# Performance work log

Hardware: AMD Instinct MI355X
Metric: run time of the kernel (lower is better)

Reference implementation:

```python
import jax, jax.numpy as jnp
import numpy as np
import math

B, T, D = 4, 2048, 1024
N, D_OUT = 1024, 1024
EPS_A = 1e-4
PROJ_BOUND = 1.0


def setup_inputs() -> dict:
    key = jax.random.key(0)
    ks = jax.random.split(key, 4)
    # reset_parameters: rho=0.99, delta0=1.0
    rho, delta0 = 0.99, 1.0
    alpha0 = -math.log(rho) / delta0
    alpha_log_val = math.log(math.expm1(alpha0))
    delta_bias_val = math.log(math.expm1(delta0))
    return {
        "u": jax.random.normal(ks[0], (B, T, D), dtype=jnp.float32),
        "z0": jnp.zeros((B, N), dtype=jnp.float32),
        "W_in_raw": 0.02 * jax.random.normal(ks[1], (N, D), dtype=jnp.float32),
        "W_out_raw": 0.02 * jax.random.normal(ks[2], (D_OUT, N), dtype=jnp.float32),
        "pn_w": 0.02 * jax.random.normal(ks[3], (3 * N, D), dtype=jnp.float32),
        "pn_b": jnp.zeros((3 * N,), dtype=jnp.float32),
        "alpha_log": jnp.full((N,), alpha_log_val, dtype=jnp.float32),
        "delta_bias": jnp.full((N,), delta_bias_val, dtype=jnp.float32),
        "log_gamma": jnp.float32(0.0),
    }


def _bounded_linear(x, W, bound):
    # y = x @ (W/scale)^T with ||W/scale||_2 <= bound (exact spectral norm)
    sigma = jnp.maximum(jnp.linalg.norm(W, ord=2), 1e-5)
    scale = jnp.maximum(sigma / bound, 1.0)
    return x @ (W / scale).T


def reference(u, z0, W_in_raw, W_out_raw, pn_w, pn_b, alpha_log, delta_bias, log_gamma):
    g = jnp.exp(log_gamma)
    u_scaled = g * _bounded_linear(u, W_in_raw, PROJ_BOUND)        # (B,T,N)
    raw = u @ pn_w.T + pn_b                                        # (B,T,3N)
    delta_raw, b_raw, c_raw = jnp.split(raw, 3, axis=-1)
    delta = jax.nn.softplus(delta_raw + delta_bias)
    alpha = jax.nn.softplus(alpha_log)                             # (N,)
    a = jnp.minimum(jnp.exp(-delta * alpha), 1.0 - EPS_A)          # (B,T,N)
    b = jnp.tanh(b_raw)
    c = jnp.tanh(c_raw)
    # exact spectral norm of [[a,b],[c,0]] per coordinate
    p = a * a + c * c
    r = b * b
    q = a * b
    disc = (p - r) * (p - r) + 4.0 * q * q
    lam_max = 0.5 * (p + r + jnp.sqrt(disc + 1e-12))
    sigma = jnp.sqrt(lam_max + 1e-12)
    scale = jnp.maximum(sigma, 1.0)
    a, b, c = a / scale, b / scale, c / scale
    # diagonal recurrence z_{t+1} = a_t * z_t + b_t * u_scaled_t via associative scan
    bu = b * u_scaled
    bu = bu.at[:, 0].add(a[:, 0] * z0)
    def combine(x, y):
        a1, b1 = x
        a2, b2 = y
        return (a2 * a1, a2 * b1 + b2)
    _, z_next = jax.lax.associative_scan(combine, (a, bu), axis=1)  # z_1..z_T (B,T,N)
    # y_t = W_out (c_t * z_t) with z_t = state BEFORE update (one-step delay)
    states = jnp.concatenate([z0[:, None, :], z_next[:, :-1, :]], axis=1)  # z_0..z_{T-1}
    y_hat = c * states
    y = _bounded_linear(y_hat, W_out_raw, PROJ_BOUND)              # (B,T,D_out)
    return y
```

## Files before the change

kernel.cpp:

```cpp
#include <hip/hip_runtime.h>
#include <stdint.h>

#define B_ 4
#define T_ 2048
#define D_ 1024
#define N_ 1024
#define TC 16
#define NCH (T_/TC)
#define SQN 6

typedef __attribute__((ext_vector_type(4))) float f32x4;
typedef __attribute__((ext_vector_type(8))) short bf16x8;
typedef __attribute__((ext_vector_type(4))) unsigned short us4;

__device__ __forceinline__ unsigned short f2bf(float f){
  unsigned int u = __float_as_uint(f);
  return (unsigned short)((u + 0x7fffu + ((u >> 16) & 1u)) >> 16);
}
__device__ __forceinline__ float bf2f(unsigned short h){
  return __uint_as_float(((unsigned int)h) << 16);
}

__device__ __forceinline__ float inv_scale(const float* __restrict__ sc, int z){
  float ll = 0.f, w = 1.f, t = 1.f;
  #pragma unroll
  for (int i = 0; i <= SQN; i++){
    t = sc[8 + 2*i + z];
    ll += w * __logf(t);
    w *= 0.5f;
  }
  float F = sc[8 + 2*(SQN+1) + z];
  ll += w * __logf(F / (t*t));
  float sig = fmaxf(__expf(0.5f * ll), 1e-5f);
  return 1.f / fmaxf(sig, 1.f);
}

__device__ __forceinline__ float softplusf(float x){
  return (x > 0.f) ? (x + __logf(1.f + __expf(-x))) : __logf(1.f + __expf(x));
}
__device__ __forceinline__ float tanhfastf(float x){
  float e = __expf(2.f * x);
  return 1.f - 2.f/(e + 1.f);
}
__device__ __forceinline__ float tanhrcpf(float x){
  float e = __expf(2.f * x);
  return 1.f - 2.f*__builtin_amdgcn_rcpf(e + 1.f);
}

#define U4    2097152
#define WIN4   262144
#define PNW4   786432
#define WOUT4  262144
#define CONV_BLOCKS ((U4 + WIN4 + PNW4 + WOUT4 + 255)/256)

__global__ void k_convert_all(const float* __restrict__ u, const float* __restrict__ Win,
                              const float* __restrict__ pnw, const float* __restrict__ Wout,
                              unsigned short* __restrict__ u16, unsigned short* __restrict__ Wcat16,
                              unsigned short* __restrict__ Wout16, float* __restrict__ sc){
  if (blockIdx.x == 0 && threadIdx.x < 64) sc[threadIdx.x] = 0.f;
  long i = (long)blockIdx.x * 256 + threadIdx.x;
  const float* src; long o; size_t didx; unsigned short* dbuf;
  if (i < U4){
    src = u; o = i; dbuf = u16; didx = (size_t)o;
  } else if (i < U4+WIN4){
    o = i - U4; src = Win;
    int n = (int)(o >> 8), c4 = (int)(o & 255);
    dbuf = Wcat16; didx = (size_t)(4*n)*256 + c4;
  } else if (i < U4+WIN4+PNW4){
    o = i - (U4+WIN4); src = pnw;
    int m = (int)(o >> 8), c4 = (int)(o & 255);
    int s = (m >> 10) + 1, n = m & 1023;
    dbuf = Wcat16; didx = (size_t)(4*n + s)*256 + c4;
  } else if (i < U4+WIN4+PNW4+WOUT4){
    o = i - (U4+WIN4+PNW4); src = Wout; dbuf = Wout16; didx = (size_t)o;
  } else return;
  float4 v = ((const float4*)src)[o];
  us4 w;
  w.x = f2bf(v.x); w.y = f2bf(v.y); w.z = f2bf(v.z); w.w = f2bf(v.w);
  ((us4*)dbuf)[didx] = w;
}

__device__ __forceinline__ void load_lds16(const unsigned short* g, unsigned short* l){
  __builtin_amdgcn_global_load_lds((const __attribute__((address_space(1))) void*)g,
                                   (__attribute__((address_space(3))) void*)l, 16, 0, 0);
}

__global__ __launch_bounds__(256) void k_pgemm(
    const unsigned short* __restrict__ A,
    const unsigned short* __restrict__ Bmat,
    const float* __restrict__ alog, const float* __restrict__ dbias,
    const float* __restrict__ pnb, const float* __restrict__ lgam,
    const float* __restrict__ sc,
    unsigned int* __restrict__ G1,
    float* __restrict__ G2,
    float* __restrict__ Asum, float* __restrict__ Ssum)
{
  __shared__ alignas(16) char smem[36864];
  unsigned short* As = (unsigned short*)smem;
  unsigned short* Bs = (unsigned short*)(smem + 16384);
  const int tid = threadIdx.x;
  const int wid = tid >> 6;
  const int lane = tid & 63;
  const int bn = blockIdx.x, bm = blockIdx.y;
  const int K = 1024;

  const int wr = wid >> 1, wc = wid & 1;
  const int rg = lane >> 3;
  const int cby = (lane & 7) << 4;
  const int srow0 = wid * 32;
  const int frow = lane & 15;
  const int kgrp = lane >> 4;

  const unsigned short* ap[4];
  const unsigned short* bp[4];
  unsigned short* adst[4];
  unsigned short* bdst[4];
  #pragma unroll
  for (int i = 0; i < 4; i++){
    int r = srow0 + i*8 + rg;
    int cb = cby ^ ((r & 7) << 4);
    ap[i] = A    + (size_t)(bm*128 + r)*K + (cb >> 1);
    bp[i] = Bmat + (size_t)(bn*128 + r)*K + (cb >> 1);
    adst[i] = As + (srow0 + i*8)*64;
    bdst[i] = Bs + (srow0 + i*8)*64;
  }
  int aoff[4][2], boff[4][2];
  #pragma unroll
  for (int m = 0; m < 4; m++){
    int r = wr*64 + m*16 + frow;
    #pragma unroll
    for (int kk = 0; kk < 2; kk++)
      aoff[m][kk] = r*128 + ((kk*64 + kgrp*16) ^ ((r & 7) << 4));
  }
  #pragma unroll
  for (int n2 = 0; n2 < 4; n2++){
    int r = wc*64 + n2*16 + frow;
    #pragma unroll
    for (int kk = 0; kk < 2; kk++)
      boff[n2][kk] = r*128 + ((kk*64 + kgrp*16) ^ ((r & 7) << 4));
  }

  f32x4 acc[4][4] = {};

  for (int kt = 0; kt < K; kt += 64){
    #pragma unroll
    for (int i = 0; i < 4; i++){
      load_lds16(ap[i], adst[i]);
      load_lds16(bp[i], bdst[i]);
      ap[i] += 64; bp[i] += 64;
    }
    __syncthreads();
    #pragma unroll
    for (int kk = 0; kk < 2; kk++){
      bf16x8 af[4], bfv[4];
      #pragma unroll
      for (int m = 0; m < 4; m++)
        af[m] = *(const bf16x8*)((const char*)As + aoff[m][kk]);
      #pragma unroll
      for (int n2 = 0; n2 < 4; n2++)
        bfv[n2] = *(const bf16x8*)((const char*)Bs + boff[n2][kk]);
      #pragma unroll
      for (int m = 0; m < 4; m++)
        #pragma unroll
        for (int n2 = 0; n2 < 4; n2++)
          acc[m][n2] = __builtin_amdgcn_mfma_f32_16x16x32_bf16(bfv[n2], af[m], acc[m][n2], 0, 0, 0);
    }
    __syncthreads();
  }

  unsigned int* g1s = (unsigned int*)smem;
  float*        g2s = (float*)(smem + 18432);

  const float ginv = __expf(lgam[0]) * inv_scale(sc, 0);
  float alpha[4], bd[4], bb[4], bc[4];
  #pragma unroll
  for (int nw = 0; nw < 4; nw++){
    int n = bn*32 + wc*16 + nw*4 + kgrp;
    alpha[nw] = softplusf(alog[n]);
    bd[nw] = dbias[n] + pnb[n];
    bb[nw] = pnb[N_ + n];
    bc[nw] = pnb[2*N_ + n];
  }
  #pragma unroll
  for (int mu = 0; mu < 4; mu++){
    const int tl = wr*64 + mu*16 + frow;
    #pragma unroll
    for (int nw = 0; nw < 4; nw++){
      const int nl = wc*16 + nw*4 + kgrp;
      f32x4 v = acc[mu][nw];
      float lp = __logf(1.f + __expf(v[1] + bd[nw]));
      float av = fminf(__expf(-alpha[nw]*lp), 1.f - 1e-4f);
      float bv = tanhrcpf(v[2] + bb[nw]);
      float cv = tanhrcpf(v[3] + bc[nw]);
      float p = av*av + cv*cv;
      float r = bv*bv;
      float q = av*bv;
      float pr = p - r;
      float disc = pr*pr + 4.f*q*q;
      float lam = 0.5f*(p + r + sqrtf(disc + 1e-12f));
      float inv = fminf(rsqrtf(lam + 1e-12f), 1.f);
      float a = av * inv;
      float c = cv * inv;
      float bu = (bv * inv) * (v[0] * ginv);
      g1s[tl*36 + nl] = (unsigned int)f2bf(a) | ((unsigned int)f2bf(c) << 16);
      g2s[tl*36 + nl] = bu;
    }
  }
  __syncthreads();
  const size_t t0b = (size_t)bm * 128;
  const int nb = bn*32;
  #pragma unroll
  for (int r = 0; r < 4; r++){
    int flat = r*256 + tid;
    int tl = flat >> 3, seg = flat & 7;
    uint4  v1 = *(const uint4*)(g1s + tl*36 + seg*4);
    float4 v2 = *(const float4*)(g2s + tl*36 + seg*4);
    *(uint4*)(G1 + (t0b + tl)*N_ + nb + seg*4) = v1;
    *(float4*)(G2 + (t0b + tl)*N_ + nb + seg*4) = v2;
  }
  {
    const int chl = tid >> 5;
    const int nl  = tid & 31;
    float Ar = 1.f, Sr = 0.f;
    #pragma unroll
    for (int i = 0; i < 16; i++){
      int row = chl*16 + i;
      float a = bf2f((unsigned short)(g1s[row*36 + nl] & 0xffffu));
      float bu = g2s[row*36 + nl];
      Sr = fmaf(a, Sr, bu);
      Ar *= a;
    }
    const size_t gch = (size_t)bm*8 + chl;
    Asum[gch*N_ + nb + nl] = Ar;
    Ssum[gch*N_ + nb + nl] = Sr;
  }
}

template<int OUTBF16>
__global__ __launch_bounds__(256) void k_gemm(
    const unsigned short* __restrict__ A,
    const unsigned short* __restrict__ Bmat,
    void* __restrict__ C0,
    int M, int N, int K,
    const float* __restrict__ sc, int step)
{
  __shared__ alignas(16) unsigned short As[128*64];
  __shared__ alignas(16) unsigned short Bs[128*64];
  const int tid = threadIdx.x;
  const int wid = tid >> 6;
  const int lane = tid & 63;
  const int bn = blockIdx.x, bm = blockIdx.y;

  char* C = (char*)C0;
  float outscale = (step >= 0) ? inv_scale(sc, step) : 1.f;

  const int wr = wid >> 1, wc = wid & 1;
  const int rg = lane >> 3;
  const int cby = (lane & 7) << 4;
  const int srow0 = wid * 32;
  const int frow = lane & 15;
  const int kgrp = lane >> 4;

  const unsigned short* ap[4];
  const unsigned short* bp[4];
  unsigned short* adst[4];
  unsigned short* bdst[4];
  #pragma unroll
  for (int i = 0; i < 4; i++){
    int r = srow0 + i*8 + rg;
    int cb = cby ^ ((r & 7) << 4);
    ap[i] = A    + (size_t)(bm*128 + r)*K + (cb >> 1);
    bp[i] = Bmat + (size_t)(bn*128 + r)*K + (cb >> 1);
    adst[i] = As + (srow0 + i*8)*64;
    bdst[i] = Bs + (srow0 + i*8)*64;
  }
  int aoff[4][2], boff[4][2];
  #pragma unroll
  for (int m = 0; m < 4; m++){
    int r = wr*64 + m*16 + frow;
    #pragma unroll
    for (int kk = 0; kk < 2; kk++)
      aoff[m][kk] = r*128 + ((kk*64 + kgrp*16) ^ ((r & 7) << 4));
  }
  #pragma unroll
  for (int n2 = 0; n2 < 4; n2++){
    int r = wc*64 + n2*16 + frow;
    #pragma unroll
    for (int kk = 0; kk < 2; kk++)
      boff[n2][kk] = r*128 + ((kk*64 + kgrp*16) ^ ((r & 7) << 4));
  }

  f32x4 acc[4][4] = {};

  for (int kt = 0; kt < K; kt += 64){
    #pragma unroll
    for (int i = 0; i < 4; i++){
      load_lds16(ap[i], adst[i]);
      load_lds16(bp[i], bdst[i]);
      ap[i] += 64; bp[i] += 64;
    }
    __syncthreads();
    #pragma unroll
    for (int kk = 0; kk < 2; kk++){
      bf16x8 af[4], bfv[4];
      #pragma unroll
      for (int m = 0; m < 4; m++)
        af[m] = *(const bf16x8*)((const char*)As + aoff[m][kk]);
      #pragma unroll
      for (int n2 = 0; n2 < 4; n2++)
        bfv[n2] = *(const bf16x8*)((const char*)Bs + boff[n2][kk]);
      #pragma unroll
      for (int m = 0; m < 4; m++)
        #pragma unroll
        for (int n2 = 0; n2 < 4; n2++)
          acc[m][n2] = __builtin_amdgcn_mfma_f32_16x16x32_bf16(af[m], bfv[n2], acc[m][n2], 0, 0, 0);
    }
    __syncthreads();
  }

  const int row0 = bm*128 + wr*64;
  const int col0 = bn*128 + wc*64 + frow;
  #pragma unroll
  for (int m = 0; m < 4; m++){
    #pragma unroll
    for (int n2 = 0; n2 < 4; n2++){
      const int col = col0 + n2*16;
      const int rb = row0 + m*16 + kgrp*4;
      #pragma unroll
      for (int j = 0; j < 4; j++){
        float v = acc[m][n2][j] * outscale;
        if (OUTBF16) ((unsigned short*)C)[(size_t)(rb + j)*N + col] = f2bf(v);
        else         ((float*)C)[(size_t)(rb + j)*N + col] = v;
      }
    }
  }
}

__global__ __launch_bounds__(256) void k_sq(
    const unsigned short* __restrict__ A0, unsigned short* __restrict__ C0,
    const unsigned short* __restrict__ A1, unsigned short* __restrict__ C1,
    float* __restrict__ sc, int step)
{
  __shared__ alignas(16) unsigned short As0[64*128], Bs0[64*128];
  __shared__ alignas(16) unsigned short As1[64*128], Bs1[64*128];
  const int tid = threadIdx.x;
  const int wid = tid >> 6;
  const int lane = tid & 63;
  const int z = blockIdx.z;

  int x = blockIdx.x, bm = 0;
  while (x >= 16 - bm){ x -= 16 - bm; bm++; }
  const int bn = bm + x;

  const unsigned short* A = z ? A1 : A0;
  unsigned short* C = z ? C1 : C0;
  const size_t rs = (step == 0 && z == 0) ? 4096 : 1024;
  float outscale = 1.f;
  if (step > 0){ float t = sc[8 + (step-1)*2 + z]; outscale = 1.f/(t*t); }

  const int wr = wid >> 1, wc = wid & 1;
  const int frow = lane & 15;
  const int kgrp = lane >> 4;

  const int srl = lane >> 4;
  const int sgr = lane & 15;
  const int swzr = wid*4 + srl;
  const int scol_e = ((sgr ^ swzr) << 3);

  const size_t Arow = (size_t)bm * 64;
  const size_t Brow = (size_t)bn * 64;

  f32x4 acc[2][2] = {};

  auto stage = [&](unsigned short* as, unsigned short* bs, int t){
    const int kt = t * 128;
    #pragma unroll
    for (int i = 0; i < 4; i++){
      int r = i*16 + wid*4 + srl;
      load_lds16(A + (Arow + r)*rs + kt + scol_e, as + (i*16 + wid*4)*128);
      load_lds16(A + (Brow + r)*rs + kt + scol_e, bs + (i*16 + wid*4)*128);
    }
  };

  auto compute = [&](const unsigned short* as, const unsigned short* bs){
    #pragma unroll
    for (int ks = 0; ks < 4; ks++){
      const int kb = ks*64 + kgrp*16;
      bf16x8 af[2], bfv[2];
      #pragma unroll
      for (int m = 0; m < 2; m++){
        int r = wr*32 + m*16 + frow;
        af[m] = *(const bf16x8*)((const char*)as + r*256 + (kb ^ (frow << 4)));
      }
      #pragma unroll
      for (int n2 = 0; n2 < 2; n2++){
        int r = wc*32 + n2*16 + frow;
        bfv[n2] = *(const bf16x8*)((const char*)bs + r*256 + (kb ^ (frow << 4)));
      }
      #pragma unroll
      for (int m = 0; m < 2; m++)
        #pragma unroll
        for (int n2 = 0; n2 < 2; n2++)
          acc[m][n2] = __builtin_amdgcn_mfma_f32_16x16x32_bf16(af[m], bfv[n2], acc[m][n2], 0, 0, 0);
    }
  };

  stage(As0, Bs0, 0);
  __syncthreads();
  for (int t2 = 0; t2 < 8; t2 += 2){
    if (t2 + 1 < 8) stage(As1, Bs1, t2 + 1);
    compute(As0, Bs0);
    __syncthreads();
    if (t2 + 2 < 8) stage(As0, Bs0, t2 + 2);
    compute(As1, Bs1);
    __syncthreads();
  }

  const int row0 = bm*64 + wr*32;
  const int col0 = bn*64 + wc*32 + frow;
  float fr = 0.f;
  #pragma unroll
  for (int m = 0; m < 2; m++){
    #pragma unroll
    for (int n2 = 0; n2 < 2; n2++){
      const int col = col0 + n2*16;
      const int rb = row0 + m*16 + kgrp*4;
      us4 tw;
      #pragma unroll
      for (int j = 0; j < 4; j++){
        float v = acc[m][n2][j] * outscale;
        unsigned short h = f2bf(v);
        C[(size_t)(rb + j)*1024 + col] = h;
        tw[j] = h;
        fr += v*v;
      }
      if (bm != bn)
        *(us4*)(C + (size_t)col*1024 + rb) = tw;
    }
  }
  if (bm == bn && wr == wc){
    int j = frow - kgrp*4;
    if (j >= 0 && j < 4){
      float d = (acc[0][0][j] + acc[1][1][j]) * outscale;
      atomicAdd(&sc[8 + step*2 + z], d);
    }
  }
  if (step == SQN){
    if (bm != bn) fr *= 2.f;
    #pragma unroll
    for (int off = 32; off; off >>= 1) fr += __shfl_down(fr, off, 64);
    if (lane == 0) atomicAdd(&sc[8 + 2*(SQN+1) + z], fr);
  }
}

__global__ __launch_bounds__(256) void k_scanB(
    const unsigned int* __restrict__ G1, const float* __restrict__ G2,
    const float* __restrict__ Asum, const float* __restrict__ Ssum,
    const float* __restrict__ z0, unsigned short* __restrict__ yh)
{
  const int tid = threadIdx.x;
  const int n0 = tid*4;
  const int ch = blockIdx.x, b = blockIdx.y;
  float z[4];
  #pragma unroll
  for (int j = 0; j < 4; j++) z[j] = z0[b*N_ + n0 + j];
  for (int c2 = 0; c2 < ch; c2++){
    const size_t idx = (size_t)(b*NCH + c2)*N_ + n0;
    float4 Av = *(const float4*)(Asum + idx);
    float4 Sv = *(const float4*)(Ssum + idx);
    z[0] = fmaf(Av.x, z[0], Sv.x);
    z[1] = fmaf(Av.y, z[1], Sv.y);
    z[2] = fmaf(Av.z, z[2], Sv.z);
    z[3] = fmaf(Av.w, z[3], Sv.w);
  }
  const size_t base = (size_t)(b*T_ + ch*TC)*N_ + n0;
  const unsigned int* g1 = G1 + base;
  const float* g2 = G2 + base;
  unsigned short* Y = yh + base;
  #pragma unroll 4
  for (int i = 0; i < TC; i++){
    uint4 pac = *(const uint4*)g1;
    float4 bu = *(const float4*)g2;
    us4 ow;
    #pragma unroll
    for (int j = 0; j < 4; j++){
      unsigned int p = j==0 ? pac.x : j==1 ? pac.y : j==2 ? pac.z : pac.w;
      float buj     = j==0 ? bu.x  : j==1 ? bu.y  : j==2 ? bu.z  : bu.w;
      float a = bf2f((unsigned short)(p & 0xffffu));
      float c = bf2f((unsigned short)(p >> 16));
      float yv = c * z[j];
      z[j] = fmaf(a, z[j], buj);
      ow[j] = f2bf(yv);
    }
    *(us4*)Y = ow;
    g1 += N_; g2 += N_; Y += N_;
  }
}

extern "C" void kernel_launch(void* const* d_in, const int* in_sizes, int n_in,
                              void* d_out, int out_size, void* d_ws, size_t ws_size,
                              hipStream_t stream)
{
  const float* u    = (const float*)d_in[0];
  const float* z0   = (const float*)d_in[1];
  const float* Win  = (const float*)d_in[2];
  const float* Wout = (const float*)d_in[3];
  const float* pnw  = (const float*)d_in[4];
  const float* pnb  = (const float*)d_in[5];
  const float* alog = (const float*)d_in[6];
  const float* dbias= (const float*)d_in[7];
  const float* lgam = (const float*)d_in[8];

  char* ws = (char*)d_ws;
  size_t off = 0;
  auto alloc = [&](size_t bytes) -> void* {
    void* p = ws + off;
    off += (bytes + 255) & ~(size_t)255;
    return p;
  };
  float*          sc     = (float*)         alloc(1024);
  unsigned short* u16    = (unsigned short*)alloc((size_t)8192*1024*2);
  unsigned short* Wcat16 = (unsigned short*)alloc((size_t)4096*1024*2);
  unsigned short* Wout16 = (unsigned short*)alloc((size_t)1024*1024*2);
  unsigned int*   G1     = (unsigned int*)  alloc((size_t)8192*1024*4);
  float*          G2     = (float*)         alloc((size_t)8192*1024*4);
  unsigned short* yh16   = (unsigned short*)alloc((size_t)8192*1024*2);
  unsigned short* Hping  = (unsigned short*)alloc((size_t)2*1024*1024*2);
  unsigned short* Hpong  = (unsigned short*)alloc((size_t)2*1024*1024*2);
  float*          Asum   = (float*)alloc((size_t)B_*NCH*N_*4);
  float*          Ssum   = (float*)alloc((size_t)B_*NCH*N_*4);

  k_convert_all<<<CONV_BLOCKS, 256, 0, stream>>>(u, Win, pnw, Wout, u16, Wcat16, Wout16, sc);

  dim3 gsq(136, 1, 2);
  k_sq<<<gsq, 256, 0, stream>>>(Wcat16, Hping, Wout16, Hping + (size_t)1024*1024, sc, 0);
  unsigned short* hin = Hping;
  unsigned short* hout = Hpong;
  for (int s = 1; s <= SQN; s++){
    k_sq<<<gsq, 256, 0, stream>>>(hin, hout, hin + (size_t)1024*1024, hout + (size_t)1024*1024, sc, s);
    unsigned short* t = hin; hin = hout; hout = t;
  }

  dim3 g1(4096/128, 8192/128);
  k_pgemm<<<g1, 256, 0, stream>>>(u16, Wcat16, alog, dbias, pnb, lgam, sc, G1, G2, Asum, Ssum);

  dim3 gb(NCH, B_);
  k_scanB<<<gb, 256, 0, stream>>>(G1, G2, Asum, Ssum, z0, yh16);

  dim3 g2(1024/128, 8192/128);
  k_gemm<0><<<g2, 256, 0, stream>>>(yh16, Wout16, d_out, 8192, 1024, 1024, sc, 1);
}
```

Before: 264.4 us.

## Precompute per-step affine coefficients in pgemm so emit pass reads one packed array

The GEMM epilogue now runs the intra-chunk scan locally and stores, for each timestep, the bf16 pair (c*prefixA, c*prefixS). The output is then an affine function of the chunk-start state, computed as y = u1*z_chunk + u2. This removes the separate fp32 bu array (32MB write plus read) and the sequential recurrence from the emit kernel. In exchange, prefix products and sums are rounded to bf16, which may reduce accuracy.

```diff
diff --git a/kernel.cpp b/kernel.cpp
--- a/kernel.cpp
+++ b/kernel.cpp
@@ -37,10 +37,6 @@
 
 __device__ __forceinline__ float softplusf(float x){
   return (x > 0.f) ? (x + __logf(1.f + __expf(-x))) : __logf(1.f + __expf(x));
-}
-__device__ __forceinline__ float tanhfastf(float x){
-  float e = __expf(2.f * x);
-  return 1.f - 2.f/(e + 1.f);
 }
 __device__ __forceinline__ float tanhrcpf(float x){
   float e = __expf(2.f * x);
@@ -91,8 +87,7 @@
     const float* __restrict__ alog, const float* __restrict__ dbias,
     const float* __restrict__ pnb, const float* __restrict__ lgam,
     const float* __restrict__ sc,
-    unsigned int* __restrict__ G1,
-    float* __restrict__ G2,
+    unsigned int* __restrict__ U,
     float* __restrict__ Asum, float* __restrict__ Ssum)
 {
   __shared__ alignas(16) char smem[36864];
@@ -207,32 +202,34 @@
     }
   }
   __syncthreads();
-  const size_t t0b = (size_t)bm * 128;
-  const int nb = bn*32;
-  #pragma unroll
-  for (int r = 0; r < 4; r++){
-    int flat = r*256 + tid;
-    int tl = flat >> 3, seg = flat & 7;
-    uint4  v1 = *(const uint4*)(g1s + tl*36 + seg*4);
-    float4 v2 = *(const float4*)(g2s + tl*36 + seg*4);
-    *(uint4*)(G1 + (t0b + tl)*N_ + nb + seg*4) = v1;
-    *(float4*)(G2 + (t0b + tl)*N_ + nb + seg*4) = v2;
-  }
   {
     const int chl = tid >> 5;
     const int nl  = tid & 31;
     float Ar = 1.f, Sr = 0.f;
     #pragma unroll
     for (int i = 0; i < 16; i++){
-      int row = chl*16 + i;
-      float a = bf2f((unsigned short)(g1s[row*36 + nl] & 0xffffu));
-      float bu = g2s[row*36 + nl];
+      int off = (chl*16 + i)*36 + nl;
+      unsigned int pk = g1s[off];
+      float a = bf2f((unsigned short)(pk & 0xffffu));
+      float c = bf2f((unsigned short)(pk >> 16));
+      float bu = g2s[off];
+      g1s[off] = (unsigned int)f2bf(c*Ar) | ((unsigned int)f2bf(c*Sr) << 16);
       Sr = fmaf(a, Sr, bu);
       Ar *= a;
     }
     const size_t gch = (size_t)bm*8 + chl;
-    Asum[gch*N_ + nb + nl] = Ar;
-    Ssum[gch*N_ + nb + nl] = Sr;
+    Asum[gch*N_ + bn*32 + nl] = Ar;
+    Ssum[gch*N_ + bn*32 + nl] = Sr;
+  }
+  __syncthreads();
+  const size_t t0b = (size_t)bm * 128;
+  const int nb = bn*32;
+  #pragma unroll
+  for (int r = 0; r < 4; r++){
+    int flat = r*256 + tid;
+    int tl = flat >> 3, seg = flat & 7;
+    uint4 v1 = *(const uint4*)(g1s + tl*36 + seg*4);
+    *(uint4*)(U + (t0b + tl)*N_ + nb + seg*4) = v1;
   }
 }
 
@@ -453,8 +450,8 @@
   }
 }
 
-__global__ __launch_bounds__(256) void k_scanB(
-    const unsigned int* __restrict__ G1, const float* __restrict__ G2,
+__global__ __launch_bounds__(256) void k_emit(
+    const unsigned int* __restrict__ U,
     const float* __restrict__ Asum, const float* __restrict__ Ssum,
     const float* __restrict__ z0, unsigned short* __restrict__ yh)
 {
@@ -474,26 +471,21 @@
     z[3] = fmaf(Av.w, z[3], Sv.w);
   }
   const size_t base = (size_t)(b*T_ + ch*TC)*N_ + n0;
-  const unsigned int* g1 = G1 + base;
-  const float* g2 = G2 + base;
+  const unsigned int* up = U + base;
   unsigned short* Y = yh + base;
   #pragma unroll 4
   for (int i = 0; i < TC; i++){
-    uint4 pac = *(const uint4*)g1;
-    float4 bu = *(const float4*)g2;
+    uint4 pac = *(const uint4*)up;
     us4 ow;
     #pragma unroll
     for (int j = 0; j < 4; j++){
       unsigned int p = j==0 ? pac.x : j==1 ? pac.y : j==2 ? pac.z : pac.w;
-      float buj     = j==0 ? bu.x  : j==1 ? bu.y  : j==2 ? bu.z  : bu.w;
-      float a = bf2f((unsigned short)(p & 0xffffu));
-      float c = bf2f((unsigned short)(p >> 16));
-      float yv = c * z[j];
-      z[j] = fmaf(a, z[j], buj);
-      ow[j] = f2bf(yv);
+      float u1 = bf2f((unsigned short)(p & 0xffffu));
+      float u2 = bf2f((unsigned short)(p >> 16));
+      ow[j] = f2bf(fmaf(u1, z[j], u2));
     }
     *(us4*)Y = ow;
-    g1 += N_; g2 += N_; Y += N_;
+    up += N_; Y += N_;
   }
 }
 
@@ -522,8 +514,7 @@
   unsigned short* u16    = (unsigned short*)alloc((size_t)8192*1024*2);
   unsigned short* Wcat16 = (unsigned short*)alloc((size_t)4096*1024*2);
   unsigned short* Wout16 = (unsigned short*)alloc((size_t)1024*1024*2);
-  unsigned int*   G1     = (unsigned int*)  alloc((size_t)8192*1024*4);
-  float*          G2     = (float*)         alloc((size_t)8192*1024*4);
+  unsigned int*   Upk    = (unsigned int*)  alloc((size_t)8192*1024*4);
   unsigned short* yh16   = (unsigned short*)alloc((size_t)8192*1024*2);
   unsigned short* Hping  = (unsigned short*)alloc((size_t)2*1024*1024*2);
   unsigned short* Hpong  = (unsigned short*)alloc((size_t)2*1024*1024*2);
@@ -542,10 +533,10 @@
   }
 
   dim3 g1(4096/128, 8192/128);
-  k_pgemm<<<g1, 256, 0, stream>>>(u16, Wcat16, alog, dbias, pnb, lgam, sc, G1, G2, Asum, Ssum);
+  k_pgemm<<<g1, 256, 0, stream>>>(u16, Wcat16, alog, dbias, pnb, lgam, sc, Upk, Asum, Ssum);
 
   dim3 gb(NCH, B_);
-  k_scanB<<<gb, 256, 0, stream>>>(G1, G2, Asum, Ssum, z0, yh16);
+  k_emit<<<gb, 256, 0, stream>>>(Upk, Asum, Ssum, z0, yh16);
 
   dim3 g2(1024/128, 8192/128);
   k_gemm<0><<<g2, 256, 0, stream>>>(yh16, Wout16, d_out, 8192, 1024, 1024, sc, 1);
```

After: 263.2 us (median of 2 runs). No clear change (-0.4%).
